# Performance work log

Hardware: AMD Instinct MI355X
Metric: run time of the kernel (lower is better)

The kernel has to match this reference:

```python
import jax, jax.numpy as jnp
import numpy as np

BATCH, SEQ, D_MODEL = 8, 4096, 1024
N, K, RHO_MAX, N_POWER_ITER = 16, 4, 0.3, 2
P = N * (N - 1) // 2  # 120 skew params


def _xavier(key, shape, gain):
    fan_out, fan_in = shape
    std = gain * np.sqrt(2.0 / (fan_in + fan_out))
    return jax.random.normal(key, shape, jnp.float32) * std


def setup_inputs() -> dict:
    key = jax.random.key(0)
    k0, k1, k2, k3 = jax.random.split(key, 4)
    u = jax.random.normal(k0, (BATCH, SEQ, D_MODEL), jnp.float32)
    W_proj_w = _xavier(k1, (P, D_MODEL), 0.1)
    W_proj_b = jnp.zeros((P,), jnp.float32)
    B_w = _xavier(k2, (N, D_MODEL), 0.5)
    C_w = _xavier(k3, (D_MODEL, N), 0.5)
    D = jnp.zeros((D_MODEL,), jnp.float32)
    return {"u": u, "W_proj_w": W_proj_w, "W_proj_b": W_proj_b, "B_w": B_w, "C_w": C_w, "D": D}


def _normalize(x, axis):
    # F.normalize: x / max(||x||, eps)
    return x / jnp.maximum(jnp.linalg.norm(x, axis=axis, keepdims=True), 1e-12)


def reference(u, W_proj_w, W_proj_b, B_w, C_w, D):
    Bsz, T, d = u.shape
    n = B_w.shape[0]
    rows, cols = np.triu_indices(n, 1)

    # 1. skew params for all timesteps at once: (B,T,P)
    v = u @ W_proj_w.T + W_proj_b
    A = jnp.zeros((Bsz, T, n, n), u.dtype)
    A = A.at[..., rows, cols].set(v).at[..., cols, rows].set(-v)

    # 2. spectral-norm scaling (power iteration runs with no grad in torch)
    A_sg = jax.lax.stop_gradient(A)
    u_vec = _normalize(jax.random.normal(jax.random.key(1), (Bsz, T, n, 1), u.dtype), axis=2)
    for _ in range(N_POWER_ITER):
        v_vec = _normalize(jnp.swapaxes(A_sg, -1, -2) @ u_vec, axis=2)
        u_vec = _normalize(A_sg @ v_vec, axis=2)
    sigma = jnp.abs((jnp.swapaxes(u_vec, -1, -2) @ (A @ v_vec))[..., 0, 0])  # (B,T)
    scale = RHO_MAX / jnp.maximum(sigma, RHO_MAX)
    A = A * scale[..., None, None]

    # 3. Neumann-Cayley, k=4 radix-2 splitting: W = (I-A)(I+A^2)(I-A)
    I = jnp.eye(n, dtype=u.dtype)
    ImA = I - A
    W = (ImA @ (I + A @ A)) @ ImA  # (B,T,n,n)

    # orthogonality deviation (monitoring, no grad)
    W_sg = jax.lax.stop_gradient(W)
    WtW = jnp.swapaxes(W_sg, -1, -2) @ W_sg
    ortho_dev = jnp.mean(jnp.linalg.norm(WtW - I, axis=(-2, -1)))

    # 4. sequential state recurrence h_t = W_t h_{t-1} + B u_t via scan
    Bx = u @ B_w.T  # (B,T,n)

    def step(h, inp):
        W_t, bx_t = inp  # (B,n,n), (B,n)
        h = jnp.einsum('bij,bj->bi', W_t, h) + bx_t
        return h, h

    h0 = jnp.zeros((Bsz, n), u.dtype)
    _, hs = jax.lax.scan(step, h0, (jnp.swapaxes(W, 0, 1), jnp.swapaxes(Bx, 0, 1)))
    h_all = jnp.swapaxes(hs, 0, 1)  # (B,T,n)

    y = h_all @ C_w.T + u * D
    return y, ortho_dev
```

## Files before the change

kernel.cpp:

```cpp
#include <hip/hip_runtime.h>
#include <hip/hip_bf16.h>
#include <math.h>

#define BATCHN 8
#define SEQN 4096
#define DMODEL 1024
#define MTOT (BATCHN*SEQN)
#define VB_STRIDE 136
#define CHUNKS 128
#define CLEN 32
#define YSIZE ((size_t)MTOT*DMODEL)
#define BN_ROWS 144

typedef __attribute__((ext_vector_type(8))) short short8;
typedef __attribute__((ext_vector_type(4))) float f32x4;

__device__ __forceinline__ unsigned short f2bf(float x){
  __hip_bfloat16 h = __float2bfloat16(x);
  return *(unsigned short*)&h;
}
__device__ __forceinline__ float bf2f(unsigned short b){
  __hip_bfloat16 h; *(unsigned short*)&h = b;
  return __bfloat162float(h);
}

__device__ __forceinline__ unsigned rotl32(unsigned x, int d){ return (x<<d)|(x>>(32-d)); }
__device__ __forceinline__ void tfr(unsigned &x0, unsigned &x1, int r){ x0 += x1; x1 = rotl32(x1,r); x1 ^= x0; }

__device__ __forceinline__ float xla_erfinv(float x){
  float w = -log1pf(-x*x);
  float p;
  if (w < 5.0f){
    w = w - 2.5f;
    p = 2.81022636e-08f;
    p = fmaf(p, w, 3.43273939e-07f);
    p = fmaf(p, w, -3.5233877e-06f);
    p = fmaf(p, w, -4.39150654e-06f);
    p = fmaf(p, w, 0.00021858087f);
    p = fmaf(p, w, -0.00125372503f);
    p = fmaf(p, w, -0.00417768164f);
    p = fmaf(p, w, 0.246640727f);
    p = fmaf(p, w, 1.50140941f);
  } else {
    w = sqrtf(w) - 3.0f;
    p = -0.000200214257f;
    p = fmaf(p, w, 0.000100950558f);
    p = fmaf(p, w, 0.00134934322f);
    p = fmaf(p, w, -0.00367342844f);
    p = fmaf(p, w, 0.00573950773f);
    p = fmaf(p, w, -0.0076224613f);
    p = fmaf(p, w, 0.00943887047f);
    p = fmaf(p, w, 1.00167406f);
    p = fmaf(p, w, 2.83297682f);
  }
  return p * x;
}

__device__ float jax_randn(unsigned I){
  unsigned x0 = 0u, x1 = I;
  const unsigned ks2 = 0x1BD11BDBu;
  x0 += 0u; x1 += 1u;
  tfr(x0,x1,13); tfr(x0,x1,15); tfr(x0,x1,26); tfr(x0,x1,6);
  x0 += 1u; x1 += ks2 + 1u;
  tfr(x0,x1,17); tfr(x0,x1,29); tfr(x0,x1,16); tfr(x0,x1,24);
  x0 += ks2; x1 += 0u + 2u;
  tfr(x0,x1,13); tfr(x0,x1,15); tfr(x0,x1,26); tfr(x0,x1,6);
  x0 += 0u; x1 += 1u + 3u;
  tfr(x0,x1,17); tfr(x0,x1,29); tfr(x0,x1,16); tfr(x0,x1,24);
  x0 += 1u; x1 += ks2 + 4u;
  tfr(x0,x1,13); tfr(x0,x1,15); tfr(x0,x1,26); tfr(x0,x1,6);
  x0 += ks2; x1 += 0u + 5u;
  unsigned bits = x0 ^ x1;
  unsigned fb = (bits >> 9) | 0x3f800000u;
  float f = __uint_as_float(fb) - 1.0f;
  const float lo = -0.99999994f;
  float val = f * 2.0f + lo;
  val = fmaxf(lo, val);
  return 1.4142135381698608f * xla_erfinv(val);
}

__global__ __launch_bounds__(256) void k0_presplit(const float* __restrict__ Wp,
    const float* __restrict__ Bw, unsigned short* __restrict__ Bhi,
    unsigned short* __restrict__ Blo){
  int i = blockIdx.x*256 + threadIdx.x;
  if (i >= BN_ROWS*DMODEL/4) return;
  int n = i >> 8;
  int k = (i & 255) * 4;
  float4 t4 = make_float4(0.f,0.f,0.f,0.f);
  if (n < 120)      t4 = *(const float4*)(Wp + (size_t)n*DMODEL + k);
  else if (n < 136) t4 = *(const float4*)(Bw + (size_t)(n-120)*DMODEL + k);
  unsigned short h[4], l[4];
  float v[4] = {t4.x,t4.y,t4.z,t4.w};
  #pragma unroll
  for (int j=0;j<4;j++){
    h[j] = f2bf(v[j]);
    l[j] = f2bf(v[j] - bf2f(h[j]));
  }
  int c  = k >> 5;
  int q  = (k >> 3) & 3;
  int jj = k & 7;
  int t  = n >> 4;
  int lr = n & 15;
  size_t off = ((((size_t)c*9 + t)*64) + q*16 + lr)*8 + jj;
  *(ushort4*)(Bhi + off) = make_ushort4(h[0],h[1],h[2],h[3]);
  *(ushort4*)(Blo + off) = make_ushort4(l[0],l[1],l[2],l[3]);
}

#define K1_THREADS 512

#define K1_LOAD(C, ARA, ARB, BH, BL) do{                                  \
  const float* _ap = aptr + (C)*32;                                       \
  ARA = *(const float4*)(_ap);                                            \
  ARB = *(const float4*)(_ap + 4);                                        \
  _Pragma("unroll")                                                       \
  for (int _t=0;_t<5;_t++){                                               \
    size_t _off = (((size_t)(C)*9 + t0 + _t)*64 + lane)*8;                \
    BH[_t] = *(const short8*)(Bhi + _off);                                \
    BL[_t] = *(const short8*)(Blo + _off);                                \
  }                                                                       \
}while(0)

#define K1_CONV(ARA, ARB, AH, AL) do{                                     \
  float _va[8] = {ARA.x,ARA.y,ARA.z,ARA.w,ARB.x,ARB.y,ARB.z,ARB.w};       \
  _Pragma("unroll")                                                       \
  for (int _j=0;_j<8;_j++){                                               \
    unsigned short _h = f2bf(_va[_j]);                                    \
    AH[_j] = (short)_h;                                                   \
    AL[_j] = (short)f2bf(_va[_j] - bf2f(_h));                             \
  }                                                                       \
}while(0)

#define K1_MM(AH, AL, BH, BL) do{                                         \
  _Pragma("unroll")                                                       \
  for (int _t=0;_t<5;_t++){                                               \
    acc[_t] = __builtin_amdgcn_mfma_f32_16x16x32_bf16(AH, BH[_t], acc[_t], 0,0,0); \
    acc[_t] = __builtin_amdgcn_mfma_f32_16x16x32_bf16(AH, BL[_t], acc[_t], 0,0,0); \
    acc[_t] = __builtin_amdgcn_mfma_f32_16x16x32_bf16(AL, BH[_t], acc[_t], 0,0,0); \
  }                                                                       \
}while(0)

__global__ __launch_bounds__(512, 4) void k1_mfma(const float* __restrict__ u,
    const unsigned short* __restrict__ Bhi, const unsigned short* __restrict__ Blo,
    const float* __restrict__ Wpb, float* __restrict__ vb){
  const int tid  = threadIdx.x;
  const int wid  = tid >> 6;
  const int lane = tid & 63;
  const int quad = lane >> 4;
  const int lrow = lane & 15;
  const int wm   = wid & 3;
  const int wn   = wid >> 2;
  const int t0   = wn ? 4 : 0;
  const int m0   = blockIdx.x * 64;

  const float* aptr = u + (size_t)(m0 + wm*16 + lrow)*DMODEL + quad*8;

  f32x4 acc[5];
  #pragma unroll
  for (int t=0;t<5;t++) acc[t] = (f32x4){0.f,0.f,0.f,0.f};

  float4 ar0a, ar0b, ar1a, ar1b;
  short8 bh0[5], bl0[5], bh1[5], bl1[5];
  short8 ah0, al0, ah1, al1;

  K1_LOAD(0, ar0a, ar0b, bh0, bl0);

  for (int c=0; c<DMODEL/32; c+=2){
    K1_LOAD(c+1, ar1a, ar1b, bh1, bl1);
    K1_CONV(ar0a, ar0b, ah0, al0);
    K1_MM(ah0, al0, bh0, bl0);
    if (c+2 < DMODEL/32)
      K1_LOAD(c+2, ar0a, ar0b, bh0, bl0);
    K1_CONV(ar1a, ar1b, ah1, al1);
    K1_MM(ah1, al1, bh1, bl1);
  }

  #pragma unroll
  for (int t=0;t<5;t++){
    if (wn == 1 && t == 0) continue;
    int col = (t0+t)*16 + lrow;
    if (col < VB_STRIDE){
      float bias = (col < 120) ? Wpb[col] : 0.f;
      #pragma unroll
      for (int i=0;i<4;i++){
        int row = m0 + wm*16 + quad*4 + i;
        vb[(size_t)row*VB_STRIDE + col] = acc[t][i] + bias;
      }
    }
  }
}

__global__ __launch_bounds__(128) void k2_build_w(const float* __restrict__ vb,
    float* __restrict__ Wg, float* __restrict__ ortho){
  __shared__ float Af[8*324];
  __shared__ float Sf[8*324];
  __shared__ float gsum[8];
  const int tid = threadIdx.x;
  const int grp = tid >> 4;
  const int r   = tid & 15;
  const int m   = blockIdx.x*8 + grp;
  float* A = Af + grp*324;
  float* S = Sf + grp*324;
  const float* vrow = vb + (size_t)m*VB_STRIDE;

  float a_s[16];
  #pragma unroll
  for (int c=0;c<16;c++){
    float val = 0.f;
    if (c > r)      val =  vrow[r*15 - (r*(r-1))/2 + (c-r-1)];
    else if (c < r) val = -vrow[c*15 - (c*(c-1))/2 + (r-c-1)];
    a_s[c] = val;
  }

  float uv = jax_randn((unsigned)m*16u + (unsigned)r);
  float nn = uv*uv;
  #pragma unroll
  for (int s=1;s<16;s<<=1) nn += __shfl_xor(nn, s, 16);
  uv = uv / fmaxf(sqrtf(nn), 1e-12f);

  float t2 = 0.f;
  #pragma unroll
  for (int it=0; it<2; ++it){
    float t1 = 0.f;
    #pragma unroll
    for (int k=0;k<16;k++) t1 += a_s[k]*__shfl(uv, k, 16);
    t1 = -t1;
    nn = t1*t1;
    #pragma unroll
    for (int s=1;s<16;s<<=1) nn += __shfl_xor(nn, s, 16);
    float vvec = t1 / fmaxf(sqrtf(nn), 1e-12f);
    t2 = 0.f;
    #pragma unroll
    for (int k=0;k<16;k++) t2 += a_s[k]*__shfl(vvec, k, 16);
    nn = t2*t2;
    #pragma unroll
    for (int s=1;s<16;s<<=1) nn += __shfl_xor(nn, s, 16);
    uv = t2 / fmaxf(sqrtf(nn), 1e-12f);
  }
  float sig = uv * t2;
  #pragma unroll
  for (int s=1;s<16;s<<=1) sig += __shfl_xor(sig, s, 16);
  sig = fabsf(sig);
  const float scale = 0.3f / fmaxf(sig, 0.3f);
  #pragma unroll
  for (int k=0;k<16;k++) a_s[k] *= scale;

  #pragma unroll
  for (int q=0;q<4;q++)
    *(float4*)(A + r*20 + q*4) = make_float4(a_s[q*4],a_s[q*4+1],a_s[q*4+2],a_s[q*4+3]);
  __syncthreads();

  float s_s[16];
  #pragma unroll
  for (int j=0;j<16;j++) s_s[j] = 0.f;
  #pragma unroll
  for (int k=0;k<16;k++){
    #pragma unroll
    for (int q=0;q<4;q++){
      float4 ak = *(const float4*)(A + k*20 + q*4);
      s_s[q*4+0] = fmaf(a_s[k], ak.x, s_s[q*4+0]);
      s_s[q*4+1] = fmaf(a_s[k], ak.y, s_s[q*4+1]);
      s_s[q*4+2] = fmaf(a_s[k], ak.z, s_s[q*4+2]);
      s_s[q*4+3] = fmaf(a_s[k], ak.w, s_s[q*4+3]);
    }
  }
  #pragma unroll
  for (int q=0;q<4;q++)
    *(float4*)(S + r*20 + q*4) = make_float4(s_s[q*4],s_s[q*4+1],s_s[q*4+2],s_s[q*4+3]);
  __syncthreads();

  float as_s[16], ss_s[16];
  #pragma unroll
  for (int j=0;j<16;j++){ as_s[j]=0.f; ss_s[j]=0.f; }
  #pragma unroll
  for (int k=0;k<16;k++){
    #pragma unroll
    for (int q=0;q<4;q++){
      float4 sk = *(const float4*)(S + k*20 + q*4);
      as_s[q*4+0] = fmaf(a_s[k], sk.x, as_s[q*4+0]);
      as_s[q*4+1] = fmaf(a_s[k], sk.y, as_s[q*4+1]);
      as_s[q*4+2] = fmaf(a_s[k], sk.z, as_s[q*4+2]);
      as_s[q*4+3] = fmaf(a_s[k], sk.w, as_s[q*4+3]);
      ss_s[q*4+0] = fmaf(s_s[k], sk.x, ss_s[q*4+0]);
      ss_s[q*4+1] = fmaf(s_s[k], sk.y, ss_s[q*4+1]);
      ss_s[q*4+2] = fmaf(s_s[k], sk.z, ss_s[q*4+2]);
      ss_s[q*4+3] = fmaf(s_s[k], sk.w, ss_s[q*4+3]);
    }
  }
  float w_s[16];
  #pragma unroll
  for (int j=0;j<16;j++){
    float wv = -2.f*a_s[j] + 2.f*s_s[j] - 2.f*as_s[j] + ss_s[j];
    if (j == r) wv += 1.f;
    w_s[j] = wv;
  }
  float4* wout = (float4*)(Wg + (size_t)m*256 + r*16);
  #pragma unroll
  for (int q=0;q<4;q++)
    wout[q] = make_float4(w_s[q*4],w_s[q*4+1],w_s[q*4+2],w_s[q*4+3]);

  __syncthreads();
  #pragma unroll
  for (int q=0;q<4;q++)
    *(float4*)(A + r*20 + q*4) = make_float4(w_s[q*4],w_s[q*4+1],w_s[q*4+2],w_s[q*4+3]);
  __syncthreads();
  float wt_s[16];
  #pragma unroll
  for (int j=0;j<16;j++) wt_s[j] = 0.f;
  #pragma unroll
  for (int k=0;k<16;k++){
    float ck = A[k*20 + r];
    #pragma unroll
    for (int q=0;q<4;q++){
      float4 wk = *(const float4*)(A + k*20 + q*4);
      wt_s[q*4+0] = fmaf(ck, wk.x, wt_s[q*4+0]);
      wt_s[q*4+1] = fmaf(ck, wk.y, wt_s[q*4+1]);
      wt_s[q*4+2] = fmaf(ck, wk.z, wt_s[q*4+2]);
      wt_s[q*4+3] = fmaf(ck, wk.w, wt_s[q*4+3]);
    }
  }
  float dev = 0.f;
  #pragma unroll
  for (int j=0;j<16;j++){
    float v = wt_s[j] - ((j==r)?1.f:0.f);
    dev += v*v;
  }
  #pragma unroll
  for (int s=1;s<16;s<<=1) dev += __shfl_xor(dev, s, 16);
  if (r==0) gsum[grp] = sqrtf(dev);
  __syncthreads();
  if (tid==0){
    float t=0.f;
    #pragma unroll
    for (int i=0;i<8;i++) t += gsum[i];
    atomicAdd(ortho, t);
  }
}

__global__ __launch_bounds__(64) void k3a_chunk_reduce(const float* __restrict__ Wg,
    const float* __restrict__ vb, double* __restrict__ Msum){
  const int chunk = blockIdx.x;
  const int b = chunk / CHUNKS, c = chunk - b*CHUNKS;
  const int lane = threadIdx.x, r = lane & 15, g = lane >> 4;
  __shared__ double Mb[2][16*20];
  __shared__ double sb[16];
  #pragma unroll
  for (int cc=0;cc<4;cc++) Mb[0][r*20 + 4*g + cc] = (r == 4*g+cc) ? 1.0 : 0.0;
  if (lane < 16) sb[lane] = 0.0;
  __syncthreads();
  const size_t mbase = (size_t)b*SEQN + (size_t)c*CLEN;
  float4 wq = *(const float4*)(Wg + mbase*256 + r*16 + 4*g);
  float bx = vb[mbase*VB_STRIDE + 120 + r];
  int p = 0;
  for (int t=0;t<CLEN;++t){
    float4 wn = make_float4(0.f,0.f,0.f,0.f); float bxn = 0.f;
    if (t+1 < CLEN){
      wn  = *(const float4*)(Wg + (mbase+t+1)*256 + r*16 + 4*g);
      bxn = vb[(mbase+t+1)*VB_STRIDE + 120 + r];
    }
    const double* M = Mb[p];
    double a0=0.0,a1=0.0,a2=0.0,a3=0.0, sacc=0.0;
    #pragma unroll
    for (int kg=0;kg<4;kg++){
      float wk0 = __shfl(wq.x, r + 16*kg);
      float wk1 = __shfl(wq.y, r + 16*kg);
      float wk2 = __shfl(wq.z, r + 16*kg);
      float wk3 = __shfl(wq.w, r + 16*kg);
      float wkv[4] = {wk0,wk1,wk2,wk3};
      #pragma unroll
      for (int e=0;e<4;e++){
        int k = 4*kg + e;
        double w = (double)wkv[e];
        const double* mrow = M + k*20 + 4*g;
        a0 = fma(w, mrow[0], a0);
        a1 = fma(w, mrow[1], a1);
        a2 = fma(w, mrow[2], a2);
        a3 = fma(w, mrow[3], a3);
        sacc = fma(w, sb[k], sacc);
      }
    }
    __syncthreads();
    double* Mn = Mb[1-p];
    Mn[r*20+4*g+0]=a0; Mn[r*20+4*g+1]=a1; Mn[r*20+4*g+2]=a2; Mn[r*20+4*g+3]=a3;
    if (g==0) sb[r] = sacc + (double)bx;
    __syncthreads();
    p ^= 1;
    wq = wn; bx = bxn;
  }
  double* out = Msum + (size_t)chunk*272;
  #pragma unroll
  for (int cc=0;cc<4;cc++) out[r*16+4*g+cc] = Mb[p][r*20+4*g+cc];
  if (lane<16) out[256+lane] = sb[lane];
}

__global__ __launch_bounds__(64) void k3b_prefix(const double* __restrict__ Msum,
    double* __restrict__ hstart){
  const int b = blockIdx.x;
  const int lane = threadIdx.x, r = lane & 15, g = lane >> 4;
  __shared__ double q[16];
  if (lane < 16) q[lane] = 0.0;
  __syncthreads();
  const double* base = Msum + (size_t)b*CHUNKS*272;
  double2 m01 = *(const double2*)(base + r*16 + 4*g);
  double2 m23 = *(const double2*)(base + r*16 + 4*g + 2);
  double sv = base[256 + r];
  for (int c=0;c<CHUNKS;++c){
    double2 n01, n23; double svn = 0.0;
    n01.x=n01.y=n23.x=n23.y=0.0;
    if (c+1 < CHUNKS){
      const double* bn = base + (size_t)(c+1)*272;
      n01 = *(const double2*)(bn + r*16 + 4*g);
      n23 = *(const double2*)(bn + r*16 + 4*g + 2);
      svn = bn[256 + r];
    }
    if (lane < 16) hstart[((size_t)b*CHUNKS + c)*16 + lane] = q[lane];
    double part = m01.x*q[4*g+0] + m01.y*q[4*g+1] + m23.x*q[4*g+2] + m23.y*q[4*g+3];
    part += __shfl_xor(part, 16);
    part += __shfl_xor(part, 32);
    __syncthreads();
    if (g==0) q[r] = part + sv;
    __syncthreads();
    m01 = n01; m23 = n23; sv = svn;
  }
}

__global__ __launch_bounds__(64) void k3c_apply(const float* __restrict__ Wg,
    const float* __restrict__ vb, const double* __restrict__ hstart,
    float* __restrict__ hout){
  const int chunk = blockIdx.x;
  const int b = chunk / CHUNKS, c = chunk - b*CHUNKS;
  const int lane = threadIdx.x, r = lane & 15, g = lane >> 4;
  __shared__ double h[16];
  if (lane < 16) h[lane] = hstart[(size_t)chunk*16 + lane];
  __syncthreads();
  const size_t mbase = (size_t)b*SEQN + (size_t)c*CLEN;
  float4 wq = *(const float4*)(Wg + mbase*256 + r*16 + 4*g);
  float bx = vb[mbase*VB_STRIDE + 120 + r];
  for (int t=0;t<CLEN;++t){
    float4 wn = make_float4(0.f,0.f,0.f,0.f); float bxn = 0.f;
    if (t+1 < CLEN){
      wn  = *(const float4*)(Wg + (mbase+t+1)*256 + r*16 + 4*g);
      bxn = vb[(mbase+t+1)*VB_STRIDE + 120 + r];
    }
    double part = (double)wq.x*h[4*g+0] + (double)wq.y*h[4*g+1]
                + (double)wq.z*h[4*g+2] + (double)wq.w*h[4*g+3];
    part += __shfl_xor(part, 16);
    part += __shfl_xor(part, 32);
    __syncthreads();
    if (g==0){
      double nh = part + (double)bx;
      h[r] = nh;
      hout[(mbase+t)*16 + r] = (float)nh;
    }
    __syncthreads();
    wq = wn; bx = bxn;
  }
}

__device__ __forceinline__ float dot4f(float4 a, float4 b){
  return a.x*b.x + a.y*b.y + a.z*b.z + a.w*b.w;
}

__global__ __launch_bounds__(256) void k4_out(const float* __restrict__ hbuf,
    const float* __restrict__ u, const float* __restrict__ Cw,
    const float* __restrict__ D, const float* __restrict__ ortho,
    float* __restrict__ y, int write_ortho){
  __shared__ float hl[256];
  const int m0 = blockIdx.x * 16;
  hl[threadIdx.x] = hbuf[(size_t)m0*16 + threadIdx.x];
  __syncthreads();
  const int col = threadIdx.x * 4;
  float4 cm[4][4];
  #pragma unroll
  for (int cc=0;cc<4;cc++)
    #pragma unroll
    for (int jj=0;jj<4;jj++)
      cm[cc][jj] = *(const float4*)(Cw + (size_t)(col+cc)*16 + jj*4);
  float4 d4 = *(const float4*)(D + col);
  #pragma unroll
  for (int row=0;row<16;row++){
    const float4* hr = (const float4*)(hl + row*16);
    float4 h0=hr[0], h1=hr[1], h2=hr[2], h3=hr[3];
    float4 o;
    o.x = dot4f(cm[0][0],h0)+dot4f(cm[0][1],h1)+dot4f(cm[0][2],h2)+dot4f(cm[0][3],h3);
    o.y = dot4f(cm[1][0],h0)+dot4f(cm[1][1],h1)+dot4f(cm[1][2],h2)+dot4f(cm[1][3],h3);
    o.z = dot4f(cm[2][0],h0)+dot4f(cm[2][1],h1)+dot4f(cm[2][2],h2)+dot4f(cm[2][3],h3);
    o.w = dot4f(cm[3][0],h0)+dot4f(cm[3][1],h1)+dot4f(cm[3][2],h2)+dot4f(cm[3][3],h3);
    size_t off = (size_t)(m0+row)*DMODEL + col;
    float4 u4 = *(const float4*)(u + off);
    o.x += u4.x*d4.x; o.y += u4.y*d4.y; o.z += u4.z*d4.z; o.w += u4.w*d4.w;
    *(float4*)(y + off) = o;
  }
  if (write_ortho && blockIdx.x==0 && threadIdx.x==0)
    y[YSIZE] = ortho[0] * (1.0f/32768.0f);
}

extern "C" void kernel_launch(void* const* d_in, const int* in_sizes, int n_in,
                              void* d_out, int out_size, void* d_ws, size_t ws_size,
                              hipStream_t stream){
  const float* u   = (const float*)d_in[0];
  const float* Wp  = (const float*)d_in[1];
  const float* Wpb = (const float*)d_in[2];
  const float* Bw  = (const float*)d_in[3];
  const float* Cw  = (const float*)d_in[4];
  const float* D   = (const float*)d_in[5];
  float* y = (float*)d_out;

  float* f      = (float*)d_ws;
  float* vb     = f;
  float* Wg     = vb  + (size_t)MTOT*VB_STRIDE;
  float* hbuf   = Wg  + (size_t)MTOT*256;
  double* Msum  = (double*)(hbuf + (size_t)MTOT*16);
  double* hstart= Msum + (size_t)BATCHN*CHUNKS*272;
  unsigned short* Bhi = (unsigned short*)(hstart + (size_t)BATCHN*CHUNKS*16);
  unsigned short* Blo = Bhi + (size_t)BN_ROWS*DMODEL;
  float* ortho  = (float*)(Blo + (size_t)BN_ROWS*DMODEL);

  int write_ortho = ((size_t)out_size > YSIZE) ? 1 : 0;

  hipMemsetAsync(ortho, 0, sizeof(float), stream);
  hipLaunchKernelGGL(k0_presplit,     dim3((BN_ROWS*DMODEL/4+255)/256), dim3(256), 0, stream, Wp, Bw, Bhi, Blo);
  hipLaunchKernelGGL(k1_mfma,         dim3(MTOT/64), dim3(K1_THREADS), 0, stream, u, Bhi, Blo, Wpb, vb);
  hipLaunchKernelGGL(k2_build_w,      dim3(MTOT/8), dim3(128), 0, stream, vb, Wg, ortho);
  hipLaunchKernelGGL(k3a_chunk_reduce,dim3(BATCHN*CHUNKS), dim3(64), 0, stream, Wg, vb, Msum);
  hipLaunchKernelGGL(k3b_prefix,      dim3(BATCHN), dim3(64), 0, stream, Msum, hstart);
  hipLaunchKernelGGL(k3c_apply,       dim3(BATCHN*CHUNKS), dim3(64), 0, stream, Wg, vb, hstart, hbuf);
  hipLaunchKernelGGL(k4_out,          dim3(MTOT/16), dim3(256), 0, stream, hbuf, u, Cw, D, ortho, y, write_ortho);
}
```

Before: 569.0 us.

## Stage projection weight fragments through LDS with async global-to-LDS loads

The projection GEMM kernel now stages each 32-wide K-slice of the split bf16 hi/lo weight matrix into double-buffered shared memory, using direct global-to-LDS loads. Previously every wave fetched its own B fragments from global memory into registers. The presplit kernel writes a new unit-major layout to match, and the column-tile split between the two wave groups changes from an overlapping 5+5 to a 5+4 division. The aim is to cut redundant global/L2 traffic for the weights and register pressure. In exchange it adds block-wide barriers per slice and about 36KB of LDS per block, which may limit occupancy.

```diff
diff --git a/kernel.cpp b/kernel.cpp
--- a/kernel.cpp
+++ b/kernel.cpp
@@ -11,6 +11,7 @@
 #define CLEN 32
 #define YSIZE ((size_t)MTOT*DMODEL)
 #define BN_ROWS 144
+#define K1_UNITS 1152
 
 typedef __attribute__((ext_vector_type(8))) short short8;
 typedef __attribute__((ext_vector_type(4))) float f32x4;
@@ -22,6 +23,13 @@
 __device__ __forceinline__ float bf2f(unsigned short b){
   __hip_bfloat16 h; *(unsigned short*)&h = b;
   return __bfloat162float(h);
+}
+
+__device__ __forceinline__ void gload16(unsigned short* lds, const unsigned short* g){
+  __builtin_amdgcn_global_load_lds(
+      (const __attribute__((address_space(1))) unsigned int*)g,
+      (__attribute__((address_space(3))) unsigned int*)lds,
+      16, 0, 0);
 }
 
 __device__ __forceinline__ unsigned rotl32(unsigned x, int d){ return (x<<d)|(x>>(32-d)); }
@@ -80,8 +88,7 @@
 }
 
 __global__ __launch_bounds__(256) void k0_presplit(const float* __restrict__ Wp,
-    const float* __restrict__ Bw, unsigned short* __restrict__ Bhi,
-    unsigned short* __restrict__ Blo){
+    const float* __restrict__ Bw, unsigned short* __restrict__ Bfrag){
   int i = blockIdx.x*256 + threadIdx.x;
   if (i >= BN_ROWS*DMODEL/4) return;
   int n = i >> 8;
@@ -99,49 +106,58 @@
   int c  = k >> 5;
   int q  = (k >> 3) & 3;
   int jj = k & 7;
-  int t  = n >> 4;
-  int lr = n & 15;
-  size_t off = ((((size_t)c*9 + t)*64) + q*16 + lr)*8 + jj;
-  *(ushort4*)(Bhi + off) = make_ushort4(h[0],h[1],h[2],h[3]);
-  *(ushort4*)(Blo + off) = make_ushort4(l[0],l[1],l[2],l[3]);
+  size_t base = (size_t)c*K1_UNITS*8;
+  *(ushort4*)(Bfrag + base + (size_t)(n*4+q)*8 + jj)        = make_ushort4(h[0],h[1],h[2],h[3]);
+  *(ushort4*)(Bfrag + base + (size_t)((n+144)*4+q)*8 + jj)  = make_ushort4(l[0],l[1],l[2],l[3]);
 }
 
 #define K1_THREADS 512
 
-#define K1_LOAD(C, ARA, ARB, BH, BL) do{                                  \
-  const float* _ap = aptr + (C)*32;                                       \
-  ARA = *(const float4*)(_ap);                                            \
-  ARB = *(const float4*)(_ap + 4);                                        \
-  _Pragma("unroll")                                                       \
-  for (int _t=0;_t<5;_t++){                                               \
-    size_t _off = (((size_t)(C)*9 + t0 + _t)*64 + lane)*8;                \
-    BH[_t] = *(const short8*)(Bhi + _off);                                \
-    BL[_t] = *(const short8*)(Blo + _off);                                \
-  }                                                                       \
+#define K1_STAGE(C, BUF) do{                                                   \
+  const unsigned short* _gB = Bfrag + (size_t)(C)*(K1_UNITS*8);                \
+  unsigned short* _l = &Bs[BUF][0];                                            \
+  gload16(_l + (wid*64)*8,      _gB + (size_t)(tid)*8);                        \
+  gload16(_l + (wid*64+512)*8,  _gB + (size_t)(tid+512)*8);                    \
+  if (wid < 2)                                                                 \
+    gload16(_l + (wid*64+1024)*8, _gB + (size_t)(tid+1024)*8);                 \
 }while(0)
 
-#define K1_CONV(ARA, ARB, AH, AL) do{                                     \
-  float _va[8] = {ARA.x,ARA.y,ARA.z,ARA.w,ARB.x,ARB.y,ARB.z,ARB.w};       \
-  _Pragma("unroll")                                                       \
-  for (int _j=0;_j<8;_j++){                                               \
-    unsigned short _h = f2bf(_va[_j]);                                    \
-    AH[_j] = (short)_h;                                                   \
-    AL[_j] = (short)f2bf(_va[_j] - bf2f(_h));                             \
-  }                                                                       \
+#define K1_ALOAD(C, ARA, ARB) do{                                              \
+  const float* _ap = aptr + (C)*32;                                            \
+  ARA = *(const float4*)(_ap);                                                 \
+  ARB = *(const float4*)(_ap + 4);                                             \
 }while(0)
 
-#define K1_MM(AH, AL, BH, BL) do{                                         \
-  _Pragma("unroll")                                                       \
-  for (int _t=0;_t<5;_t++){                                               \
-    acc[_t] = __builtin_amdgcn_mfma_f32_16x16x32_bf16(AH, BH[_t], acc[_t], 0,0,0); \
-    acc[_t] = __builtin_amdgcn_mfma_f32_16x16x32_bf16(AH, BL[_t], acc[_t], 0,0,0); \
-    acc[_t] = __builtin_amdgcn_mfma_f32_16x16x32_bf16(AL, BH[_t], acc[_t], 0,0,0); \
-  }                                                                       \
+#define K1_COMPUTE(BUF, ARA, ARB) do{                                          \
+  short8 _ah, _al;                                                             \
+  {                                                                            \
+    float _va[8] = {ARA.x,ARA.y,ARA.z,ARA.w,ARB.x,ARB.y,ARB.z,ARB.w};          \
+    _Pragma("unroll")                                                          \
+    for (int _j=0;_j<8;_j++){                                                  \
+      unsigned short _h = f2bf(_va[_j]);                                       \
+      _ah[_j] = (short)_h;                                                     \
+      _al[_j] = (short)f2bf(_va[_j] - bf2f(_h));                               \
+    }                                                                          \
+  }                                                                            \
+  const unsigned short* _sb = &Bs[BUF][0];                                     \
+  _Pragma("unroll")                                                            \
+  for (int _t=0;_t<5;_t++){                                                    \
+    if (_t < nt){                                                              \
+      int _row = (t0+_t)*16 + lrow;                                            \
+      short8 _bh = *(const short8*)(_sb + _row*32 + quad*8);                   \
+      short8 _bl = *(const short8*)(_sb + (_row+144)*32 + quad*8);             \
+      acc[_t] = __builtin_amdgcn_mfma_f32_16x16x32_bf16(_ah, _bh, acc[_t], 0,0,0); \
+      acc[_t] = __builtin_amdgcn_mfma_f32_16x16x32_bf16(_ah, _bl, acc[_t], 0,0,0); \
+      acc[_t] = __builtin_amdgcn_mfma_f32_16x16x32_bf16(_al, _bh, acc[_t], 0,0,0); \
+    }                                                                          \
+  }                                                                            \
 }while(0)
 
 __global__ __launch_bounds__(512, 4) void k1_mfma(const float* __restrict__ u,
-    const unsigned short* __restrict__ Bhi, const unsigned short* __restrict__ Blo,
+    const unsigned short* __restrict__ Bfrag,
     const float* __restrict__ Wpb, float* __restrict__ vb){
+  __shared__ unsigned short Bs[2][K1_UNITS*8];
+
   const int tid  = threadIdx.x;
   const int wid  = tid >> 6;
   const int lane = tid & 63;
@@ -149,7 +165,8 @@
   const int lrow = lane & 15;
   const int wm   = wid & 3;
   const int wn   = wid >> 2;
-  const int t0   = wn ? 4 : 0;
+  const int t0   = wn ? 5 : 0;
+  const int nt   = wn ? 4 : 5;
   const int m0   = blockIdx.x * 64;
 
   const float* aptr = u + (size_t)(m0 + wm*16 + lrow)*DMODEL + quad*8;
@@ -158,32 +175,36 @@
   #pragma unroll
   for (int t=0;t<5;t++) acc[t] = (f32x4){0.f,0.f,0.f,0.f};
 
-  float4 ar0a, ar0b, ar1a, ar1b;
-  short8 bh0[5], bl0[5], bh1[5], bl1[5];
-  short8 ah0, al0, ah1, al1;
-
-  K1_LOAD(0, ar0a, ar0b, bh0, bl0);
+  float4 a0a, a0b, a1a, a1b;
+
+  K1_STAGE(0, 0);
+  K1_ALOAD(0, a0a, a0b);
+  __syncthreads();
 
   for (int c=0; c<DMODEL/32; c+=2){
-    K1_LOAD(c+1, ar1a, ar1b, bh1, bl1);
-    K1_CONV(ar0a, ar0b, ah0, al0);
-    K1_MM(ah0, al0, bh0, bl0);
-    if (c+2 < DMODEL/32)
-      K1_LOAD(c+2, ar0a, ar0b, bh0, bl0);
-    K1_CONV(ar1a, ar1b, ah1, al1);
-    K1_MM(ah1, al1, bh1, bl1);
+    K1_STAGE(c+1, 1);
+    K1_ALOAD(c+1, a1a, a1b);
+    K1_COMPUTE(0, a0a, a0b);
+    __syncthreads();
+    if (c+2 < DMODEL/32){
+      K1_STAGE(c+2, 0);
+      K1_ALOAD(c+2, a0a, a0b);
+    }
+    K1_COMPUTE(1, a1a, a1b);
+    if (c+2 < DMODEL/32) __syncthreads();
   }
 
   #pragma unroll
   for (int t=0;t<5;t++){
-    if (wn == 1 && t == 0) continue;
-    int col = (t0+t)*16 + lrow;
-    if (col < VB_STRIDE){
-      float bias = (col < 120) ? Wpb[col] : 0.f;
-      #pragma unroll
-      for (int i=0;i<4;i++){
-        int row = m0 + wm*16 + quad*4 + i;
-        vb[(size_t)row*VB_STRIDE + col] = acc[t][i] + bias;
+    if (t < nt){
+      int col = (t0+t)*16 + lrow;
+      if (col < VB_STRIDE){
+        float bias = (col < 120) ? Wpb[col] : 0.f;
+        #pragma unroll
+        for (int i=0;i<4;i++){
+          int row = m0 + wm*16 + quad*4 + i;
+          vb[(size_t)row*VB_STRIDE + col] = acc[t][i] + bias;
+        }
       }
     }
   }
@@ -511,15 +532,14 @@
   float* hbuf   = Wg  + (size_t)MTOT*256;
   double* Msum  = (double*)(hbuf + (size_t)MTOT*16);
   double* hstart= Msum + (size_t)BATCHN*CHUNKS*272;
-  unsigned short* Bhi = (unsigned short*)(hstart + (size_t)BATCHN*CHUNKS*16);
-  unsigned short* Blo = Bhi + (size_t)BN_ROWS*DMODEL;
-  float* ortho  = (float*)(Blo + (size_t)BN_ROWS*DMODEL);
+  unsigned short* Bfrag = (unsigned short*)(hstart + (size_t)BATCHN*CHUNKS*16);
+  float* ortho  = (float*)(Bfrag + (size_t)32*K1_UNITS*8);
 
   int write_ortho = ((size_t)out_size > YSIZE) ? 1 : 0;
 
   hipMemsetAsync(ortho, 0, sizeof(float), stream);
-  hipLaunchKernelGGL(k0_presplit,     dim3((BN_ROWS*DMODEL/4+255)/256), dim3(256), 0, stream, Wp, Bw, Bhi, Blo);
-  hipLaunchKernelGGL(k1_mfma,         dim3(MTOT/64), dim3(K1_THREADS), 0, stream, u, Bhi, Blo, Wpb, vb);
+  hipLaunchKernelGGL(k0_presplit,     dim3((BN_ROWS*DMODEL/4+255)/256), dim3(256), 0, stream, Wp, Bw, Bfrag);
+  hipLaunchKernelGGL(k1_mfma,         dim3(MTOT/64), dim3(K1_THREADS), 0, stream, u, Bfrag, Wpb, vb);
   hipLaunchKernelGGL(k2_build_w,      dim3(MTOT/8), dim3(128), 0, stream, vb, Wg, ortho);
   hipLaunchKernelGGL(k3a_chunk_reduce,dim3(BATCHN*CHUNKS), dim3(64), 0, stream, Wg, vb, Msum);
   hipLaunchKernelGGL(k3b_prefix,      dim3(BATCHN), dim3(64), 0, stream, Msum, hstart);
```

Result: faster. 467.1 us (-17.9%).
